# Kernel optimization log

Hardware: AMD Instinct MI355X
Metric: run time of the kernel (lower is better)

## Reference

```python
import jax, jax.numpy as jnp
import numpy as np

EPS = 1e-6


def _build_cayley():
    # Blade ordering of the CEGNN CliffordAlgebra for Cl(3,0): combinations order
    # 1, e1, e2, e3, e12, e13, e23, e123. Metric (1,1,1) => e_k^2 = +1.
    blades = [(), (0,), (1,), (2,), (0, 1), (0, 2), (1, 2), (0, 1, 2)]
    index = {b: i for i, b in enumerate(blades)}
    cayley = np.zeros((8, 8, 8), dtype=np.float32)
    for i, a in enumerate(blades):
        for j, b in enumerate(blades):
            arr = list(a) + list(b)
            sign = 1
            # bubble sort, counting transpositions of anticommuting generators
            for p in range(len(arr)):
                for q in range(len(arr) - 1):
                    if arr[q] > arr[q + 1]:
                        arr[q], arr[q + 1] = arr[q + 1], arr[q]
                        sign = -sign
            # contract equal adjacent generators (e_k e_k = +1)
            out = []
            q = 0
            while q < len(arr):
                if q + 1 < len(arr) and arr[q] == arr[q + 1]:
                    q += 2
                else:
                    out.append(arr[q])
                    q += 1
            cayley[i, j, index[tuple(out)]] = sign
    return cayley


_CAYLEY = jnp.asarray(_build_cayley())  # (8, 8, 8)


def _mvlinear(x, W, b):
    # MVLinear(subspaces=False): channel mixing shared across blades,
    # bias embedded into the scalar (grade-0) blade only.
    y = jnp.einsum("bmi,nm->bni", x, W)
    return y.at[:, :, 0].add(b)


def setup_inputs() -> dict:
    key = jax.random.key(0)
    ks = jax.random.split(key, 7)
    B, Cin, Ch, Cout = 16384, 512, 512, 512
    s = 1.0 / np.sqrt(Cin)
    return {
        "vec1": jax.random.normal(ks[0], (B, Cin, 8), dtype=jnp.float32),
        "W_left": jax.random.normal(ks[1], (Ch, Cin), dtype=jnp.float32) * s,
        "b_left": jax.random.normal(ks[2], (Ch,), dtype=jnp.float32) * 0.01,
        "W_right": jax.random.normal(ks[3], (Ch, Cin), dtype=jnp.float32) * s,
        "b_right": jax.random.normal(ks[4], (Ch,), dtype=jnp.float32) * 0.01,
        "W_out": jax.random.normal(ks[5], (Cout, Ch), dtype=jnp.float32) * s,
        "b_out": jax.random.normal(ks[6], (Cout,), dtype=jnp.float32) * 0.01,
        "a_norm": jnp.ones((Cout,), dtype=jnp.float32),
    }


def reference(vec1, W_left, b_left, W_right, b_right, W_out, b_out, a_norm):
    vec_right = _mvlinear(vec1, W_right, b_right)   # (B, Ch, 8)
    vec_left = _mvlinear(vec1, W_left, b_left)      # (B, Ch, 8)
    # geometric product via the sparse Cayley table of Cl(3,0)
    gp = jnp.einsum("bmi,ijk,bmj->bmk", vec_left, _CAYLEY, vec_right)
    out = _mvlinear(gp, W_out, b_out)               # (B, Cout, 8)
    # MVLayerNorm: per-multivector quadratic-form norm (all-positive metric =>
    # sqrt of sum of squared blade coefficients), averaged over channels.
    norm = jnp.sqrt(jnp.sum(out * out, axis=-1, keepdims=True))  # (B, Cout, 1)
    norm = jnp.mean(norm, axis=1, keepdims=True) + EPS           # (B, 1, 1)
    return a_norm[None, :, None] * out / norm
```

## Files before the change

kernel.cpp:

```cpp
#include <hip/hip_runtime.h>
#include <cstdint>
#include <cstddef>

typedef _Float16 f16;
typedef __attribute__((ext_vector_type(8))) _Float16 f16x8;
typedef __attribute__((ext_vector_type(2))) _Float16 f16x2;
typedef __attribute__((ext_vector_type(4))) float f32x4;

#define MFMA_F16(a, b, c) __builtin_amdgcn_mfma_f32_16x16x32_f16((a), (b), (c), 0, 0, 0)

__global__ void k0_cvt(const float* __restrict__ wl, const float* __restrict__ wr,
                       const float* __restrict__ wo, f16* __restrict__ dst) {
    int i = blockIdx.x * 256 + threadIdx.x;
    dst[i]          = (f16)wl[i];
    dst[262144 + i] = (f16)wr[i];
    dst[524288 + i] = (f16)wo[i];
}

__global__ __launch_bounds__(512, 4) void k1_gp(
    const float* __restrict__ x, const f16* __restrict__ wf,
    const float* __restrict__ bl_p, const float* __restrict__ br_p,
    char* gp_out)
{
    __shared__ __align__(16) f16 As[2][8][32*32];
    __shared__ __align__(16) f16 Ws[2][2][64*32];

    const int L   = blockIdx.x;
    const int xcd = L & 7, sl = L >> 3;
    const int bt  = xcd * 64 + (sl >> 3);
    const int ct  = sl & 7;
    const int b0  = bt * 32;
    const int n0  = ct * 64;

    const int tid  = threadIdx.x;
    const int lane = tid & 63;
    const int wv   = tid >> 6;
    const int wb   = wv >> 2, wn = wv & 3;
    const int r_lo = lane & 15, s_hi = lane >> 4;

    f32x4 accL[8], accR[8];
    const f32x4 zero = {0.f, 0.f, 0.f, 0.f};
#pragma unroll
    for (int i = 0; i < 8; ++i) { accL[i] = zero; accR[i] = zero; }

    const int sbb = tid >> 4, smg = tid & 15;
    const int abase = sbb * 32 + (((smg >> 2) ^ (sbb & 3)) << 3) + ((2 * smg) & 7);
    const int wside = tid >> 8, wnl = (tid >> 2) & 63, wc = tid & 3;
    const int wbase = wnl * 32 + ((wc ^ (wnl & 3)) << 3);
    const float* xsrc0 = x + ((size_t)(b0 + sbb) * 512 + 2 * smg) * 8;
    const f16*   wsrc0 = wf + (size_t)wside * (512 * 512) + (size_t)(n0 + wnl) * 512 + wc * 8;

    auto stage = [&](int kk, int buf) {
        const float* src = xsrc0 + (size_t)kk * 256;
        f32x4 a0 = *(const f32x4*)(src);
        f32x4 a1 = *(const f32x4*)(src + 4);
        f32x4 a2 = *(const f32x4*)(src + 8);
        f32x4 a3 = *(const f32x4*)(src + 12);
#pragma unroll
        for (int i = 0; i < 4; ++i) {
            f16x2 p; p[0] = (f16)a0[i]; p[1] = (f16)a2[i];
            *(f16x2*)&As[buf][i][abase] = p;
            f16x2 q; q[0] = (f16)a1[i]; q[1] = (f16)a3[i];
            *(f16x2*)&As[buf][i + 4][abase] = q;
        }
        f16x8 w8 = *(const f16x8*)(wsrc0 + kk * 32);
        *(f16x8*)&Ws[buf][wside][wbase] = w8;
    };

    const int ar   = wb * 16 + r_lo;
    const int aoff = ar * 32 + ((s_hi ^ (ar & 3)) << 3);
    const int nloc = wn * 16 + r_lo;
    const int boff = nloc * 32 + ((s_hi ^ (nloc & 3)) << 3);

    stage(0, 0);
    for (int kk = 0; kk < 16; ++kk) {
        __syncthreads();
        if (kk < 15) stage(kk + 1, (kk + 1) & 1);
        const int buf = kk & 1;
        f16x8 bL = *(const f16x8*)&Ws[buf][0][boff];
        f16x8 bR = *(const f16x8*)&Ws[buf][1][boff];
#pragma unroll
        for (int i = 0; i < 8; ++i) {
            f16x8 a = *(const f16x8*)&As[buf][i][aoff];
            accL[i] = MFMA_F16(a, bL, accL[i]);
            accR[i] = MFMA_F16(a, bR, accR[i]);
        }
    }

    const int n_g = n0 + nloc;
    const float blv = bl_p[n_g], brv = br_p[n_g];
#pragma unroll
    for (int rr = 0; rr < 4; ++rr) {
        const int b_g = b0 + wb * 16 + s_hi * 4 + rr;
        float Lv[8], Rv[8];
#pragma unroll
        for (int i = 0; i < 8; ++i) { Lv[i] = accL[i][rr]; Rv[i] = accR[i][rr]; }
        Lv[0] += blv; Rv[0] += brv;
        float g[8];
        g[0] = Lv[0]*Rv[0]+Lv[1]*Rv[1]+Lv[2]*Rv[2]+Lv[3]*Rv[3]-Lv[4]*Rv[4]-Lv[5]*Rv[5]-Lv[6]*Rv[6]-Lv[7]*Rv[7];
        g[1] = Lv[0]*Rv[1]+Lv[1]*Rv[0]-Lv[2]*Rv[4]-Lv[3]*Rv[5]+Lv[4]*Rv[2]+Lv[5]*Rv[3]-Lv[6]*Rv[7]-Lv[7]*Rv[6];
        g[2] = Lv[0]*Rv[2]+Lv[1]*Rv[4]+Lv[2]*Rv[0]-Lv[3]*Rv[6]-Lv[4]*Rv[1]+Lv[5]*Rv[7]+Lv[6]*Rv[3]+Lv[7]*Rv[5];
        g[3] = Lv[0]*Rv[3]+Lv[1]*Rv[5]+Lv[2]*Rv[6]+Lv[3]*Rv[0]-Lv[4]*Rv[7]-Lv[5]*Rv[1]-Lv[6]*Rv[2]-Lv[7]*Rv[4];
        g[4] = Lv[0]*Rv[4]+Lv[1]*Rv[2]-Lv[2]*Rv[1]+Lv[3]*Rv[7]+Lv[4]*Rv[0]-Lv[5]*Rv[6]+Lv[6]*Rv[5]+Lv[7]*Rv[3];
        g[5] = Lv[0]*Rv[5]+Lv[1]*Rv[3]-Lv[2]*Rv[7]-Lv[3]*Rv[1]+Lv[4]*Rv[6]+Lv[5]*Rv[0]-Lv[6]*Rv[4]-Lv[7]*Rv[2];
        g[6] = Lv[0]*Rv[6]+Lv[1]*Rv[7]+Lv[2]*Rv[3]-Lv[3]*Rv[2]-Lv[4]*Rv[5]+Lv[5]*Rv[4]+Lv[6]*Rv[0]+Lv[7]*Rv[1];
        g[7] = Lv[0]*Rv[7]+Lv[1]*Rv[6]-Lv[2]*Rv[5]+Lv[3]*Rv[4]+Lv[4]*Rv[3]-Lv[5]*Rv[2]+Lv[6]*Rv[1]+Lv[7]*Rv[0];
        char* dst = gp_out + (size_t)b_g * 16384 + (size_t)n_g * 2;
#pragma unroll
        for (int i = 0; i < 8; ++i) *(f16*)(dst + (size_t)i * 1024) = (f16)g[i];
    }
}

__global__ __launch_bounds__(1024, 4) void k2_out(
    const char* gp_in, const f16* __restrict__ wo,
    const float* __restrict__ bo_p, const float* __restrict__ an_p,
    float* outp)
{
    __shared__ __align__(16) f16 As[2][8][16*32];
    __shared__ __align__(16) f16 Bs[2][512*32];
    __shared__ float red[16][16];

    const int b0   = blockIdx.x * 16;
    const int tid  = threadIdx.x;
    const int lane = tid & 63;
    const int wv   = tid >> 6;
    const int r_lo = lane & 15, s_hi = lane >> 4;

    f32x4 acc[2][8];
    const f32x4 zero = {0.f, 0.f, 0.f, 0.f};
#pragma unroll
    for (int st = 0; st < 2; ++st)
#pragma unroll
        for (int i = 0; i < 8; ++i) acc[st][i] = zero;

    const int ablade = tid >> 6, arow = (tid >> 2) & 15, ac = tid & 3;
    const char* asrc0 = gp_in + (size_t)(b0 + arow) * 16384 + ablade * 1024 + ac * 16;
    const int aw = arow * 32 + ((ac ^ (arow & 3)) << 3);
    const int brow = tid >> 1, bc2 = (tid & 1) * 2;
    const f16* bsrc0 = wo + (size_t)brow * 512 + bc2 * 8;
    const int bw0 = brow * 32 + (((bc2    ) ^ (brow & 3)) << 3);
    const int bw1 = brow * 32 + (((bc2 + 1) ^ (brow & 3)) << 3);

    auto stage = [&](int kk, int buf) {
        if (tid < 512) {
            f16x8 v = *(const f16x8*)(asrc0 + (size_t)kk * 64);
            *(f16x8*)&As[buf][ablade][aw] = v;
        }
        const f16* bs = bsrc0 + kk * 32;
        f16x8 v0 = *(const f16x8*)(bs);
        f16x8 v1 = *(const f16x8*)(bs + 8);
        *(f16x8*)&Bs[buf][bw0] = v0;
        *(f16x8*)&Bs[buf][bw1] = v1;
    };

    const int nl0 = wv * 32 + r_lo, nl1 = nl0 + 16;
    const int boff0 = nl0 * 32 + ((s_hi ^ (nl0 & 3)) << 3);
    const int boff1 = nl1 * 32 + ((s_hi ^ (nl1 & 3)) << 3);
    const int aoff  = r_lo * 32 + ((s_hi ^ (r_lo & 3)) << 3);

    stage(0, 0);
    for (int kk = 0; kk < 16; ++kk) {
        __syncthreads();
        if (kk < 15) stage(kk + 1, (kk + 1) & 1);
        const int buf = kk & 1;
        f16x8 bf0 = *(const f16x8*)&Bs[buf][boff0];
        f16x8 bf1 = *(const f16x8*)&Bs[buf][boff1];
#pragma unroll
        for (int i = 0; i < 8; ++i) {
            f16x8 a = *(const f16x8*)&As[buf][i][aoff];
            acc[0][i] = MFMA_F16(a, bf0, acc[0][i]);
            acc[1][i] = MFMA_F16(a, bf1, acc[1][i]);
        }
    }

    const float bo0 = bo_p[nl0], bo1 = bo_p[nl1];
    const float an0 = an_p[nl0], an1 = an_p[nl1];

    float partial[4];
#pragma unroll
    for (int rr = 0; rr < 4; ++rr) {
        float o = acc[0][0][rr] + bo0;
        float ss = o * o;
#pragma unroll
        for (int i = 1; i < 8; ++i) ss += acc[0][i][rr] * acc[0][i][rr];
        float s = sqrtf(ss);
        o = acc[1][0][rr] + bo1;
        ss = o * o;
#pragma unroll
        for (int i = 1; i < 8; ++i) ss += acc[1][i][rr] * acc[1][i][rr];
        partial[rr] = s + sqrtf(ss);
    }
#pragma unroll
    for (int off = 1; off < 16; off <<= 1) {
#pragma unroll
        for (int rr = 0; rr < 4; ++rr) partial[rr] += __shfl_xor(partial[rr], off);
    }
    if (r_lo == 0) {
#pragma unroll
        for (int rr = 0; rr < 4; ++rr) red[s_hi * 4 + rr][wv] = partial[rr];
    }
    __syncthreads();

#pragma unroll
    for (int rr = 0; rr < 4; ++rr) {
        float tot = 0.f;
#pragma unroll
        for (int w = 0; w < 16; ++w) tot += red[s_hi * 4 + rr][w];
        const float inv = 1.0f / (tot * (1.0f / 512.0f) + 1e-6f);
        const float sc0 = an0 * inv, sc1 = an1 * inv;
        const int b_g = b0 + s_hi * 4 + rr;
        float* dst = outp + (size_t)b_g * 4096;
        f32x4 v;
        v[0] = (acc[0][0][rr] + bo0) * sc0;
        v[1] = acc[0][1][rr] * sc0;
        v[2] = acc[0][2][rr] * sc0;
        v[3] = acc[0][3][rr] * sc0;
        *(f32x4*)(dst + (size_t)nl0 * 8) = v;
        v[0] = acc[0][4][rr] * sc0;
        v[1] = acc[0][5][rr] * sc0;
        v[2] = acc[0][6][rr] * sc0;
        v[3] = acc[0][7][rr] * sc0;
        *(f32x4*)(dst + (size_t)nl0 * 8 + 4) = v;
        v[0] = (acc[1][0][rr] + bo1) * sc1;
        v[1] = acc[1][1][rr] * sc1;
        v[2] = acc[1][2][rr] * sc1;
        v[3] = acc[1][3][rr] * sc1;
        *(f32x4*)(dst + (size_t)nl1 * 8) = v;
        v[0] = acc[1][4][rr] * sc1;
        v[1] = acc[1][5][rr] * sc1;
        v[2] = acc[1][6][rr] * sc1;
        v[3] = acc[1][7][rr] * sc1;
        *(f32x4*)(dst + (size_t)nl1 * 8 + 4) = v;
    }
}

extern "C" void kernel_launch(void* const* d_in, const int* in_sizes, int n_in,
                              void* d_out, int out_size, void* d_ws, size_t ws_size,
                              hipStream_t stream) {
    const float* x  = (const float*)d_in[0];
    const float* wl = (const float*)d_in[1];
    const float* bl = (const float*)d_in[2];
    const float* wr = (const float*)d_in[3];
    const float* br = (const float*)d_in[4];
    const float* wo = (const float*)d_in[5];
    const float* bo = (const float*)d_in[6];
    const float* an = (const float*)d_in[7];
    f16* wf = (f16*)d_ws;

    hipLaunchKernelGGL(k0_cvt, dim3(1024), dim3(256), 0, stream, wl, wr, wo, wf);
    hipLaunchKernelGGL(k1_gp,  dim3(4096), dim3(512), 0, stream, x, wf, bl, br, (char*)d_out);
    hipLaunchKernelGGL(k2_out, dim3(1024), dim3(1024), 0, stream,
                       (const char*)d_out, wf + 524288, bo, an, (float*)d_out);
}
```

Measured before the change: 445.8 us.

## Add workspace-backed GEMM kernels streaming weights from registers with separate gp buffer

Adds new k1f/k2f kernels used when the workspace is large enough. The geometric product intermediate goes to a dedicated f16 workspace buffer instead of aliasing the output. k1f keeps only the converted activations in double-buffered LDS and loads weight fragments directly from global into registers, prefetching one k-step ahead. k2f loads both operands straight from global into registers with no LDS and fuses bias, norm reduction and scaling. The aim is less LDS traffic and synchronisation, at the cost of more global/L2 reads and register pressure, plus a dependence on the workspace size.

```diff
diff --git a/kernel.cpp b/kernel.cpp
--- a/kernel.cpp
+++ b/kernel.cpp
@@ -4,6 +4,7 @@
 
 typedef _Float16 f16;
 typedef __attribute__((ext_vector_type(8))) _Float16 f16x8;
+typedef __attribute__((ext_vector_type(4))) _Float16 f16x4;
 typedef __attribute__((ext_vector_type(2))) _Float16 f16x2;
 typedef __attribute__((ext_vector_type(4))) float f32x4;
 
@@ -15,6 +16,232 @@
     dst[i]          = (f16)wl[i];
     dst[262144 + i] = (f16)wr[i];
     dst[524288 + i] = (f16)wo[i];
+}
+
+__global__ __launch_bounds__(256, 2) void k1f(
+    const float* __restrict__ x, const f16* __restrict__ wf,
+    const float* __restrict__ bl_p, const float* __restrict__ br_p,
+    f16* __restrict__ gp)
+{
+    __shared__ __align__(16) f16 As[2][8192];
+
+    const int L = blockIdx.x;
+    const int xcd = L & 7, sl = L >> 3;
+    const int bt = xcd * 64 + (sl >> 3), ct = sl & 7;
+    const int b0 = bt * 32, n0 = ct * 64;
+
+    const int tid = threadIdx.x, lane = tid & 63, wv = tid >> 6;
+    const int wb = wv >> 1, wn = wv & 1;
+    const int r_lo = lane & 15, s_hi = lane >> 4;
+
+    const int sr = tid >> 3, sq = tid & 7;
+    const float* xsrc = x + (size_t)(b0 + sr) * 4096 + sq * 32;
+    const int wbase = sr * 32 + ((((sq >> 1)) ^ (sr & 3)) << 3) + ((sq & 1) * 4);
+
+    const int nl0 = n0 + wn * 32 + r_lo;
+    const f16* bp0 = wf + (size_t)nl0 * 512 + s_hi * 8;
+    const f16* bp1 = wf + (size_t)(nl0 + 16) * 512 + s_hi * 8;
+    const f16* bp2 = bp0 + 262144;
+    const f16* bp3 = bp1 + 262144;
+
+    const int ar = wb * 16 + r_lo;
+    const int aoff = ar * 32 + ((s_hi ^ (ar & 3)) << 3);
+
+    f32x4 accL[8][2], accR[8][2];
+    const f32x4 zero = {0.f, 0.f, 0.f, 0.f};
+#pragma unroll
+    for (int i = 0; i < 8; ++i) { accL[i][0]=zero; accL[i][1]=zero; accR[i][0]=zero; accR[i][1]=zero; }
+
+    f16x8 bcur0 = *(const f16x8*)bp0, bcur1 = *(const f16x8*)bp1;
+    f16x8 bcur2 = *(const f16x8*)bp2, bcur3 = *(const f16x8*)bp3;
+    {
+        f32x4 xa[8];
+#pragma unroll
+        for (int u = 0; u < 8; ++u) xa[u] = *(const f32x4*)(xsrc + u * 4);
+#pragma unroll
+        for (int i = 0; i < 8; ++i) {
+            f16x4 w;
+#pragma unroll
+            for (int dm = 0; dm < 4; ++dm) w[dm] = (f16)xa[dm * 2 + (i >> 2)][i & 3];
+            *(f16x4*)&As[0][i * 1024 + wbase] = w;
+        }
+    }
+    __syncthreads();
+
+#pragma unroll
+    for (int kk = 0; kk < 16; ++kk) {
+        const int buf = kk & 1;
+        f16x8 bn0, bn1, bn2, bn3;
+        f32x4 xn[8];
+        if (kk < 15) {
+            bn0 = *(const f16x8*)(bp0 + (kk + 1) * 32);
+            bn1 = *(const f16x8*)(bp1 + (kk + 1) * 32);
+            bn2 = *(const f16x8*)(bp2 + (kk + 1) * 32);
+            bn3 = *(const f16x8*)(bp3 + (kk + 1) * 32);
+#pragma unroll
+            for (int u = 0; u < 8; ++u) xn[u] = *(const f32x4*)(xsrc + (kk + 1) * 256 + u * 4);
+        }
+#pragma unroll
+        for (int i = 0; i < 8; ++i) {
+            f16x8 a = *(const f16x8*)&As[buf][i * 1024 + aoff];
+            accL[i][0] = MFMA_F16(a, bcur0, accL[i][0]);
+            accL[i][1] = MFMA_F16(a, bcur1, accL[i][1]);
+            accR[i][0] = MFMA_F16(a, bcur2, accR[i][0]);
+            accR[i][1] = MFMA_F16(a, bcur3, accR[i][1]);
+        }
+        if (kk < 15) {
+#pragma unroll
+            for (int i = 0; i < 8; ++i) {
+                f16x4 w;
+#pragma unroll
+                for (int dm = 0; dm < 4; ++dm) w[dm] = (f16)xn[dm * 2 + (i >> 2)][i & 3];
+                *(f16x4*)&As[buf ^ 1][i * 1024 + wbase] = w;
+            }
+            bcur0 = bn0; bcur1 = bn1; bcur2 = bn2; bcur3 = bn3;
+        }
+        __syncthreads();
+    }
+
+#pragma unroll
+    for (int t = 0; t < 2; ++t) {
+        const int n_g = n0 + wn * 32 + t * 16 + r_lo;
+        const float blv = bl_p[n_g], brv = br_p[n_g];
+#pragma unroll
+        for (int rr = 0; rr < 4; ++rr) {
+            const int b_g = b0 + wb * 16 + s_hi * 4 + rr;
+            float Lv[8], Rv[8];
+#pragma unroll
+            for (int i = 0; i < 8; ++i) { Lv[i] = accL[i][t][rr]; Rv[i] = accR[i][t][rr]; }
+            Lv[0] += blv; Rv[0] += brv;
+            float g[8];
+            g[0] = Lv[0]*Rv[0]+Lv[1]*Rv[1]+Lv[2]*Rv[2]+Lv[3]*Rv[3]-Lv[4]*Rv[4]-Lv[5]*Rv[5]-Lv[6]*Rv[6]-Lv[7]*Rv[7];
+            g[1] = Lv[0]*Rv[1]+Lv[1]*Rv[0]-Lv[2]*Rv[4]-Lv[3]*Rv[5]+Lv[4]*Rv[2]+Lv[5]*Rv[3]-Lv[6]*Rv[7]-Lv[7]*Rv[6];
+            g[2] = Lv[0]*Rv[2]+Lv[1]*Rv[4]+Lv[2]*Rv[0]-Lv[3]*Rv[6]-Lv[4]*Rv[1]+Lv[5]*Rv[7]+Lv[6]*Rv[3]+Lv[7]*Rv[5];
+            g[3] = Lv[0]*Rv[3]+Lv[1]*Rv[5]+Lv[2]*Rv[6]+Lv[3]*Rv[0]-Lv[4]*Rv[7]-Lv[5]*Rv[1]-Lv[6]*Rv[2]-Lv[7]*Rv[4];
+            g[4] = Lv[0]*Rv[4]+Lv[1]*Rv[2]-Lv[2]*Rv[1]+Lv[3]*Rv[7]+Lv[4]*Rv[0]-Lv[5]*Rv[6]+Lv[6]*Rv[5]+Lv[7]*Rv[3];
+            g[5] = Lv[0]*Rv[5]+Lv[1]*Rv[3]-Lv[2]*Rv[7]-Lv[3]*Rv[1]+Lv[4]*Rv[6]+Lv[5]*Rv[0]-Lv[6]*Rv[4]-Lv[7]*Rv[2];
+            g[6] = Lv[0]*Rv[6]+Lv[1]*Rv[7]+Lv[2]*Rv[3]-Lv[3]*Rv[2]-Lv[4]*Rv[5]+Lv[5]*Rv[4]+Lv[6]*Rv[0]+Lv[7]*Rv[1];
+            g[7] = Lv[0]*Rv[7]+Lv[1]*Rv[6]-Lv[2]*Rv[5]+Lv[3]*Rv[4]+Lv[4]*Rv[3]-Lv[5]*Rv[2]+Lv[6]*Rv[1]+Lv[7]*Rv[0];
+            f16* dst = gp + (size_t)b_g * 4096 + n_g;
+#pragma unroll
+            for (int i = 0; i < 8; ++i) dst[i * 512] = (f16)g[i];
+        }
+    }
+}
+
+__global__ __launch_bounds__(512, 2) void k2f(
+    const f16* __restrict__ gp, const f16* __restrict__ wo,
+    const float* __restrict__ bo_p, const float* __restrict__ an_p,
+    float* __restrict__ outp)
+{
+    __shared__ float red[16][8];
+
+    const int b0 = blockIdx.x * 16;
+    const int tid = threadIdx.x, lane = tid & 63, wv = tid >> 6;
+    const int r_lo = lane & 15, s_hi = lane >> 4;
+
+    const f16* ap0 = gp + (size_t)(b0 + r_lo) * 4096 + s_hi * 8;
+    const f16* ap1 = ap0 + 2048;
+    const f16* bq0 = wo + (size_t)(wv * 64 + r_lo) * 512 + s_hi * 8;
+    const f16* bq1 = bq0 + 16 * 512;
+    const f16* bq2 = bq0 + 32 * 512;
+    const f16* bq3 = bq0 + 48 * 512;
+
+    f32x4 acc[8][4];
+    const f32x4 zero = {0.f, 0.f, 0.f, 0.f};
+#pragma unroll
+    for (int i = 0; i < 8; ++i)
+#pragma unroll
+        for (int t = 0; t < 4; ++t) acc[i][t] = zero;
+
+    f16x8 aA[8], bB[4];
+#pragma unroll
+    for (int i = 0; i < 4; ++i) {
+        aA[i]     = *(const f16x8*)(ap0 + i * 512);
+        aA[i + 4] = *(const f16x8*)(ap1 + i * 512);
+    }
+    bB[0] = *(const f16x8*)bq0; bB[1] = *(const f16x8*)bq1;
+    bB[2] = *(const f16x8*)bq2; bB[3] = *(const f16x8*)bq3;
+
+#pragma unroll
+    for (int kk = 0; kk < 16; ++kk) {
+        f16x8 aN[8], bN[4];
+        if (kk < 15) {
+            const int o = (kk + 1) * 32;
+#pragma unroll
+            for (int i = 0; i < 4; ++i) {
+                aN[i]     = *(const f16x8*)(ap0 + i * 512 + o);
+                aN[i + 4] = *(const f16x8*)(ap1 + i * 512 + o);
+            }
+            bN[0] = *(const f16x8*)(bq0 + o); bN[1] = *(const f16x8*)(bq1 + o);
+            bN[2] = *(const f16x8*)(bq2 + o); bN[3] = *(const f16x8*)(bq3 + o);
+        }
+#pragma unroll
+        for (int i = 0; i < 8; ++i) {
+            acc[i][0] = MFMA_F16(aA[i], bB[0], acc[i][0]);
+            acc[i][1] = MFMA_F16(aA[i], bB[1], acc[i][1]);
+            acc[i][2] = MFMA_F16(aA[i], bB[2], acc[i][2]);
+            acc[i][3] = MFMA_F16(aA[i], bB[3], acc[i][3]);
+        }
+        if (kk < 15) {
+#pragma unroll
+            for (int i = 0; i < 8; ++i) aA[i] = aN[i];
+#pragma unroll
+            for (int t = 0; t < 4; ++t) bB[t] = bN[t];
+        }
+    }
+
+    float bo_t[4], an_t[4];
+#pragma unroll
+    for (int t = 0; t < 4; ++t) {
+        const int c = wv * 64 + t * 16 + r_lo;
+        bo_t[t] = bo_p[c]; an_t[t] = an_p[c];
+    }
+
+    float partial[4];
+#pragma unroll
+    for (int rr = 0; rr < 4; ++rr) {
+        float sum = 0.f;
+#pragma unroll
+        for (int t = 0; t < 4; ++t) {
+            float o = acc[0][t][rr] + bo_t[t];
+            float ss = o * o;
+#pragma unroll
+            for (int i = 1; i < 8; ++i) ss += acc[i][t][rr] * acc[i][t][rr];
+            sum += sqrtf(ss);
+        }
+        partial[rr] = sum;
+    }
+#pragma unroll
+    for (int off = 1; off < 16; off <<= 1)
+#pragma unroll
+        for (int rr = 0; rr < 4; ++rr) partial[rr] += __shfl_xor(partial[rr], off);
+    if (r_lo == 0)
+#pragma unroll
+        for (int rr = 0; rr < 4; ++rr) red[s_hi * 4 + rr][wv] = partial[rr];
+    __syncthreads();
+
+#pragma unroll
+    for (int rr = 0; rr < 4; ++rr) {
+        float tot = 0.f;
+#pragma unroll
+        for (int w = 0; w < 8; ++w) tot += red[s_hi * 4 + rr][w];
+        const float inv = 1.0f / (tot * (1.0f / 512.0f) + 1e-6f);
+        const int b_g = b0 + s_hi * 4 + rr;
+        float* dst = outp + (size_t)b_g * 4096;
+#pragma unroll
+        for (int t = 0; t < 4; ++t) {
+            const float sc = an_t[t] * inv;
+            const int c = wv * 64 + t * 16 + r_lo;
+            f32x4 v0, v1;
+            v0[0] = (acc[0][t][rr] + bo_t[t]) * sc;
+            v0[1] = acc[1][t][rr] * sc; v0[2] = acc[2][t][rr] * sc; v0[3] = acc[3][t][rr] * sc;
+            v1[0] = acc[4][t][rr] * sc; v1[1] = acc[5][t][rr] * sc;
+            v1[2] = acc[6][t][rr] * sc; v1[3] = acc[7][t][rr] * sc;
+            *(f32x4*)(dst + (size_t)c * 8) = v0;
+            *(f32x4*)(dst + (size_t)c * 8 + 4) = v1;
+        }
+    }
 }
 
 __global__ __launch_bounds__(512, 4) void k1_gp(
@@ -248,7 +475,16 @@
     f16* wf = (f16*)d_ws;
 
     hipLaunchKernelGGL(k0_cvt, dim3(1024), dim3(256), 0, stream, wl, wr, wo, wf);
-    hipLaunchKernelGGL(k1_gp,  dim3(4096), dim3(512), 0, stream, x, wf, bl, br, (char*)d_out);
-    hipLaunchKernelGGL(k2_out, dim3(1024), dim3(1024), 0, stream,
-                       (const char*)d_out, wf + 524288, bo, an, (float*)d_out);
-}
+
+    const size_t need = (size_t)2 * 1024 * 1024 + (size_t)16384 * 8192;
+    if (ws_size >= need) {
+        f16* gp = wf + (1 << 20);
+        hipLaunchKernelGGL(k1f, dim3(4096), dim3(256), 0, stream, x, wf, bl, br, gp);
+        hipLaunchKernelGGL(k2f, dim3(1024), dim3(512), 0, stream,
+                           gp, wf + 524288, bo, an, (float*)d_out);
+    } else {
+        hipLaunchKernelGGL(k1_gp, dim3(4096), dim3(512), 0, stream, x, wf, bl, br, (char*)d_out);
+        hipLaunchKernelGGL(k2_out, dim3(1024), dim3(1024), 0, stream,
+                           (const char*)d_out, wf + 524288, bo, an, (float*)d_out);
+    }
+}
```

Result: slower. 694.8 us (+55.9%).

## Pre-transpose input to blade-major fp16 and stage tiles via global_load_lds

Applied to the files above, without the earlier changes.

Adds a separate pass that converts the fp32 input into fp16 blade-major planes in workspace. Both GEMM kernels then stage their A and W tiles with direct global-to-LDS loads, using a pre-swizzled source address, instead of register round-trips. The intent is to cut per-tile conversion work and VGPR traffic in the main loops. In exchange it adds an extra kernel that reads the input and writes half as many bytes back, plus a larger workspace requirement.

```diff
diff --git a/kernel.cpp b/kernel.cpp
--- a/kernel.cpp
+++ b/kernel.cpp
@@ -4,87 +4,106 @@
 
 typedef _Float16 f16;
 typedef __attribute__((ext_vector_type(8))) _Float16 f16x8;
-typedef __attribute__((ext_vector_type(2))) _Float16 f16x2;
+typedef __attribute__((ext_vector_type(4))) _Float16 f16x4;
 typedef __attribute__((ext_vector_type(4))) float f32x4;
 
 #define MFMA_F16(a, b, c) __builtin_amdgcn_mfma_f32_16x16x32_f16((a), (b), (c), 0, 0, 0)
 
-__global__ void k0_cvt(const float* __restrict__ wl, const float* __restrict__ wr,
-                       const float* __restrict__ wo, f16* __restrict__ dst) {
+#define GL2LDS(gsrc, ldst)                                                  \
+    __builtin_amdgcn_global_load_lds(                                        \
+        (const __attribute__((address_space(1))) void*)(gsrc),               \
+        (__attribute__((address_space(3))) void*)(ldst), 16, 0, 0)
+
+
+__global__ void k0w(const float* __restrict__ wl, const float* __restrict__ wr,
+                    const float* __restrict__ wo, f16* __restrict__ dst) {
     int i = blockIdx.x * 256 + threadIdx.x;
     dst[i]          = (f16)wl[i];
     dst[262144 + i] = (f16)wr[i];
     dst[524288 + i] = (f16)wo[i];
 }
 
-__global__ __launch_bounds__(512, 4) void k1_gp(
-    const float* __restrict__ x, const f16* __restrict__ wf,
+__global__ __launch_bounds__(256) void k0x(const float* __restrict__ x,
+                                           f16* __restrict__ xt) {
+    const int bid = blockIdx.x;
+    const int b   = (bid >> 1) * 4 + (threadIdx.x >> 6);
+    const int m   = (bid & 1) * 256 + (threadIdx.x & 63) * 4;
+    const float* src = x + ((size_t)b * 512 + m) * 8;
+    f32x4 v[8];
+#pragma unroll
+    for (int u = 0; u < 8; ++u) v[u] = *(const f32x4*)(src + u * 4);
+#pragma unroll
+    for (int i = 0; i < 8; ++i) {
+        f16x4 w;
+#pragma unroll
+        for (int j = 0; j < 4; ++j) w[j] = (f16)v[j * 2 + (i >> 2)][i & 3];
+        *(f16x4*)(xt + (size_t)i * 8388608 + (size_t)b * 512 + m) = w;
+    }
+}
+
+__global__ __launch_bounds__(512, 4) void k1(
+    const f16* __restrict__ xt, const f16* __restrict__ wf,
     const float* __restrict__ bl_p, const float* __restrict__ br_p,
     char* gp_out)
 {
-    __shared__ __align__(16) f16 As[2][8][32*32];
-    __shared__ __align__(16) f16 Ws[2][2][64*32];
-
-    const int L   = blockIdx.x;
+    __shared__ __align__(16) f16 AsF[2 * 8192];
+    __shared__ __align__(16) f16 WsF[2 * 4096];
+
+    const int L = blockIdx.x;
     const int xcd = L & 7, sl = L >> 3;
-    const int bt  = xcd * 64 + (sl >> 3);
-    const int ct  = sl & 7;
-    const int b0  = bt * 32;
-    const int n0  = ct * 64;
-
-    const int tid  = threadIdx.x;
-    const int lane = tid & 63;
-    const int wv   = tid >> 6;
-    const int wb   = wv >> 2, wn = wv & 3;
+    const int bt = xcd * 64 + (sl >> 3), ct = sl & 7;
+    const int b0 = bt * 32, n0 = ct * 64;
+
+    const int tid = threadIdx.x, lane = tid & 63, wv = tid >> 6;
+    const int wb = wv >> 2, wn = wv & 3;
     const int r_lo = lane & 15, s_hi = lane >> 4;
 
-    f32x4 accL[8], accR[8];
-    const f32x4 zero = {0.f, 0.f, 0.f, 0.f};
-#pragma unroll
-    for (int i = 0; i < 8; ++i) { accL[i] = zero; accR[i] = zero; }
-
-    const int sbb = tid >> 4, smg = tid & 15;
-    const int abase = sbb * 32 + (((smg >> 2) ^ (sbb & 3)) << 3) + ((2 * smg) & 7);
-    const int wside = tid >> 8, wnl = (tid >> 2) & 63, wc = tid & 3;
-    const int wbase = wnl * 32 + ((wc ^ (wnl & 3)) << 3);
-    const float* xsrc0 = x + ((size_t)(b0 + sbb) * 512 + 2 * smg) * 8;
-    const f16*   wsrc0 = wf + (size_t)wside * (512 * 512) + (size_t)(n0 + wnl) * 512 + wc * 8;
-
-    auto stage = [&](int kk, int buf) {
-        const float* src = xsrc0 + (size_t)kk * 256;
-        f32x4 a0 = *(const f32x4*)(src);
-        f32x4 a1 = *(const f32x4*)(src + 4);
-        f32x4 a2 = *(const f32x4*)(src + 8);
-        f32x4 a3 = *(const f32x4*)(src + 12);
-#pragma unroll
-        for (int i = 0; i < 4; ++i) {
-            f16x2 p; p[0] = (f16)a0[i]; p[1] = (f16)a2[i];
-            *(f16x2*)&As[buf][i][abase] = p;
-            f16x2 q; q[0] = (f16)a1[i]; q[1] = (f16)a3[i];
-            *(f16x2*)&As[buf][i + 4][abase] = q;
-        }
-        f16x8 w8 = *(const f16x8*)(wsrc0 + kk * 32);
-        *(f16x8*)&Ws[buf][wside][wbase] = w8;
-    };
-
-    const int ar   = wb * 16 + r_lo;
+    const int gA0 = tid, gA1 = tid + 512;
+    const int ba0 = gA0 >> 7, ra0 = (gA0 >> 2) & 31, ga0 = (gA0 & 3) ^ (ra0 & 3);
+    const int ba1 = gA1 >> 7, ra1 = (gA1 >> 2) & 31, ga1 = (gA1 & 3) ^ (ra1 & 3);
+    const f16* aS0 = xt + (size_t)ba0 * 8388608 + (size_t)(b0 + ra0) * 512 + ga0 * 8;
+    const f16* aS1 = xt + (size_t)ba1 * 8388608 + (size_t)(b0 + ra1) * 512 + ga1 * 8;
+    const int side = tid >> 8, wn_ = (tid >> 2) & 63, wg = (tid & 3) ^ (wn_ & 3);
+    const f16* wS = wf + (size_t)side * 262144 + (size_t)(n0 + wn_) * 512 + wg * 8;
+
+    f16* aD0 = AsF + wv * 512;
+    f16* aD1 = AsF + 4096 + wv * 512;
+    f16* wD  = WsF + wv * 512;
+
+    const int ar = wb * 16 + r_lo;
     const int aoff = ar * 32 + ((s_hi ^ (ar & 3)) << 3);
     const int nloc = wn * 16 + r_lo;
     const int boff = nloc * 32 + ((s_hi ^ (nloc & 3)) << 3);
 
-    stage(0, 0);
+    f32x4 accL[8], accR[8];
+    const f32x4 zero = {0.f, 0.f, 0.f, 0.f};
+#pragma unroll
+    for (int i = 0; i < 8; ++i) { accL[i] = zero; accR[i] = zero; }
+
+    GL2LDS(aS0, aD0);
+    GL2LDS(aS1, aD1);
+    GL2LDS(wS, wD);
+    __syncthreads();
+
     for (int kk = 0; kk < 16; ++kk) {
-        __syncthreads();
-        if (kk < 15) stage(kk + 1, (kk + 1) & 1);
         const int buf = kk & 1;
-        f16x8 bL = *(const f16x8*)&Ws[buf][0][boff];
-        f16x8 bR = *(const f16x8*)&Ws[buf][1][boff];
+        if (kk < 15) {
+            const int nb = (buf ^ 1);
+            GL2LDS(aS0 + (kk + 1) * 32, aD0 + nb * 8192);
+            GL2LDS(aS1 + (kk + 1) * 32, aD1 + nb * 8192);
+            GL2LDS(wS + (kk + 1) * 32, wD + nb * 4096);
+        }
+        const f16* Ab = AsF + buf * 8192;
+        const f16* Wb = WsF + buf * 4096;
+        f16x8 bL = *(const f16x8*)(Wb + boff);
+        f16x8 bR = *(const f16x8*)(Wb + 2048 + boff);
 #pragma unroll
         for (int i = 0; i < 8; ++i) {
-            f16x8 a = *(const f16x8*)&As[buf][i][aoff];
+            f16x8 a = *(const f16x8*)(Ab + i * 1024 + aoff);
             accL[i] = MFMA_F16(a, bL, accL[i]);
             accR[i] = MFMA_F16(a, bR, accR[i]);
         }
+        __syncthreads();
     }
 
     const int n_g = n0 + nloc;
@@ -111,66 +130,68 @@
     }
 }
 
-__global__ __launch_bounds__(1024, 4) void k2_out(
+__global__ __launch_bounds__(1024, 4) void k2(
     const char* gp_in, const f16* __restrict__ wo,
     const float* __restrict__ bo_p, const float* __restrict__ an_p,
     float* outp)
 {
-    __shared__ __align__(16) f16 As[2][8][16*32];
-    __shared__ __align__(16) f16 Bs[2][512*32];
+    __shared__ __align__(16) f16 AsF[2 * 4096];
+    __shared__ __align__(16) f16 BsF[2 * 16384];
     __shared__ float red[16][16];
 
-    const int b0   = blockIdx.x * 16;
-    const int tid  = threadIdx.x;
-    const int lane = tid & 63;
-    const int wv   = tid >> 6;
+    const int b0 = blockIdx.x * 16;
+    const int tid = threadIdx.x, lane = tid & 63, wv = tid >> 6;
     const int r_lo = lane & 15, s_hi = lane >> 4;
 
-    f32x4 acc[2][8];
-    const f32x4 zero = {0.f, 0.f, 0.f, 0.f};
-#pragma unroll
-    for (int st = 0; st < 2; ++st)
-#pragma unroll
-        for (int i = 0; i < 8; ++i) acc[st][i] = zero;
-
-    const int ablade = tid >> 6, arow = (tid >> 2) & 15, ac = tid & 3;
-    const char* asrc0 = gp_in + (size_t)(b0 + arow) * 16384 + ablade * 1024 + ac * 16;
-    const int aw = arow * 32 + ((ac ^ (arow & 3)) << 3);
-    const int brow = tid >> 1, bc2 = (tid & 1) * 2;
-    const f16* bsrc0 = wo + (size_t)brow * 512 + bc2 * 8;
-    const int bw0 = brow * 32 + (((bc2    ) ^ (brow & 3)) << 3);
-    const int bw1 = brow * 32 + (((bc2 + 1) ^ (brow & 3)) << 3);
-
-    auto stage = [&](int kk, int buf) {
-        if (tid < 512) {
-            f16x8 v = *(const f16x8*)(asrc0 + (size_t)kk * 64);
-            *(f16x8*)&As[buf][ablade][aw] = v;
-        }
-        const f16* bs = bsrc0 + kk * 32;
-        f16x8 v0 = *(const f16x8*)(bs);
-        f16x8 v1 = *(const f16x8*)(bs + 8);
-        *(f16x8*)&Bs[buf][bw0] = v0;
-        *(f16x8*)&Bs[buf][bw1] = v1;
-    };
-
+    const int gA = tid;
+    const int abl = gA >> 6, arw = (gA >> 2) & 15, agp = (gA & 3) ^ (arw & 3);
+    const char* aS = gp_in + (size_t)(b0 + arw) * 16384 + abl * 1024 + agp * 16;
+    const int gB0 = tid, gB1 = tid + 1024;
+    const int bn0 = gB0 >> 2, bg0 = (gB0 & 3) ^ (bn0 & 3);
+    const int bn1 = gB1 >> 2, bg1 = (gB1 & 3) ^ (bn1 & 3);
+    const f16* bS0 = wo + (size_t)bn0 * 512 + bg0 * 8;
+    const f16* bS1 = wo + (size_t)bn1 * 512 + bg1 * 8;
+
+    f16* aD  = AsF + wv * 512;
+    f16* bD0 = BsF + wv * 512;
+    f16* bD1 = BsF + 8192 + wv * 512;
+
+    const int aoff = r_lo * 32 + ((s_hi ^ (r_lo & 3)) << 3);
     const int nl0 = wv * 32 + r_lo, nl1 = nl0 + 16;
     const int boff0 = nl0 * 32 + ((s_hi ^ (nl0 & 3)) << 3);
     const int boff1 = nl1 * 32 + ((s_hi ^ (nl1 & 3)) << 3);
-    const int aoff  = r_lo * 32 + ((s_hi ^ (r_lo & 3)) << 3);
-
-    stage(0, 0);
+
+    f32x4 acc[2][8];
+    const f32x4 zero = {0.f, 0.f, 0.f, 0.f};
+#pragma unroll
+    for (int st = 0; st < 2; ++st)
+#pragma unroll
+        for (int i = 0; i < 8; ++i) acc[st][i] = zero;
+
+    if (wv < 8) GL2LDS(aS, aD);
+    GL2LDS(bS0, bD0);
+    GL2LDS(bS1, bD1);
+    __syncthreads();
+
     for (int kk = 0; kk < 16; ++kk) {
-        __syncthreads();
-        if (kk < 15) stage(kk + 1, (kk + 1) & 1);
         const int buf = kk & 1;
-        f16x8 bf0 = *(const f16x8*)&Bs[buf][boff0];
-        f16x8 bf1 = *(const f16x8*)&Bs[buf][boff1];
+        if (kk < 15) {
+            const int nb = buf ^ 1;
+            if (wv < 8) GL2LDS(aS + (kk + 1) * 64, aD + nb * 4096);
+            GL2LDS(bS0 + (kk + 1) * 32, bD0 + nb * 16384);
+            GL2LDS(bS1 + (kk + 1) * 32, bD1 + nb * 16384);
+        }
+        const f16* Ab = AsF + buf * 4096;
+        const f16* Bb = BsF + buf * 16384;
+        f16x8 bf0 = *(const f16x8*)(Bb + boff0);
+        f16x8 bf1 = *(const f16x8*)(Bb + boff1);
 #pragma unroll
         for (int i = 0; i < 8; ++i) {
-            f16x8 a = *(const f16x8*)&As[buf][i][aoff];
+            f16x8 a = *(const f16x8*)(Ab + i * 512 + aoff);
             acc[0][i] = MFMA_F16(a, bf0, acc[0][i]);
             acc[1][i] = MFMA_F16(a, bf1, acc[1][i]);
         }
+        __syncthreads();
     }
 
     const float bo0 = bo_p[nl0], bo1 = bo_p[nl1];
@@ -191,14 +212,12 @@
         partial[rr] = s + sqrtf(ss);
     }
 #pragma unroll
-    for (int off = 1; off < 16; off <<= 1) {
+    for (int off = 1; off < 16; off <<= 1)
 #pragma unroll
         for (int rr = 0; rr < 4; ++rr) partial[rr] += __shfl_xor(partial[rr], off);
-    }
-    if (r_lo == 0) {
+    if (r_lo == 0)
 #pragma unroll
         for (int rr = 0; rr < 4; ++rr) red[s_hi * 4 + rr][wv] = partial[rr];
-    }
     __syncthreads();
 
 #pragma unroll
@@ -212,24 +231,16 @@
         float* dst = outp + (size_t)b_g * 4096;
         f32x4 v;
         v[0] = (acc[0][0][rr] + bo0) * sc0;
-        v[1] = acc[0][1][rr] * sc0;
-        v[2] = acc[0][2][rr] * sc0;
-        v[3] = acc[0][3][rr] * sc0;
+        v[1] = acc[0][1][rr] * sc0; v[2] = acc[0][2][rr] * sc0; v[3] = acc[0][3][rr] * sc0;
         *(f32x4*)(dst + (size_t)nl0 * 8) = v;
-        v[0] = acc[0][4][rr] * sc0;
-        v[1] = acc[0][5][rr] * sc0;
-        v[2] = acc[0][6][rr] * sc0;
-        v[3] = acc[0][7][rr] * sc0;
+        v[0] = acc[0][4][rr] * sc0; v[1] = acc[0][5][rr] * sc0;
+        v[2] = acc[0][6][rr] * sc0; v[3] = acc[0][7][rr] * sc0;
         *(f32x4*)(dst + (size_t)nl0 * 8 + 4) = v;
         v[0] = (acc[1][0][rr] + bo1) * sc1;
-        v[1] = acc[1][1][rr] * sc1;
-        v[2] = acc[1][2][rr] * sc1;
-        v[3] = acc[1][3][rr] * sc1;
+        v[1] = acc[1][1][rr] * sc1; v[2] = acc[1][2][rr] * sc1; v[3] = acc[1][3][rr] * sc1;
         *(f32x4*)(dst + (size_t)nl1 * 8) = v;
-        v[0] = acc[1][4][rr] * sc1;
-        v[1] = acc[1][5][rr] * sc1;
-        v[2] = acc[1][6][rr] * sc1;
-        v[3] = acc[1][7][rr] * sc1;
+        v[0] = acc[1][4][rr] * sc1; v[1] = acc[1][5][rr] * sc1;
+        v[2] = acc[1][6][rr] * sc1; v[3] = acc[1][7][rr] * sc1;
         *(f32x4*)(dst + (size_t)nl1 * 8 + 4) = v;
     }
 }
@@ -246,9 +257,11 @@
     const float* bo = (const float*)d_in[6];
     const float* an = (const float*)d_in[7];
     f16* wf = (f16*)d_ws;
-
-    hipLaunchKernelGGL(k0_cvt, dim3(1024), dim3(256), 0, stream, wl, wr, wo, wf);
-    hipLaunchKernelGGL(k1_gp,  dim3(4096), dim3(512), 0, stream, x, wf, bl, br, (char*)d_out);
-    hipLaunchKernelGGL(k2_out, dim3(1024), dim3(1024), 0, stream,
+    f16* xt = wf + (1 << 20);
+
+    hipLaunchKernelGGL(k0w, dim3(1024), dim3(256), 0, stream, wl, wr, wo, wf);
+    hipLaunchKernelGGL(k0x, dim3(8192), dim3(256), 0, stream, x, xt);
+    hipLaunchKernelGGL(k1,  dim3(4096), dim3(512), 0, stream, xt, wf, bl, br, (char*)d_out);
+    hipLaunchKernelGGL(k2,  dim3(1024), dim3(1024), 0, stream,
                        (const char*)d_out, wf + 524288, bo, an, (float*)d_out);
 }
```

Measured after the change: 453.4 us. Within noise of the previous version (+1.7%).
